# Kernel optimization log

Hardware: AMD Instinct MI355X
Metric: run time of the kernel (lower is better)

Reference implementation:

```python
import jax, jax.numpy as jnp
import numpy as np

PATCH = 13  # fixed patch_size -> rfft bins = 13//2 + 1 = 7


def setup_inputs() -> dict:
    key = jax.random.key(0)
    k1, k2, k3 = jax.random.split(key, 3)
    B, C, n, t = 32, 64, 128, PATCH
    embed_dim = 512
    x = jax.random.normal(k1, (B, C, n, t), dtype=jnp.float32)
    # Linear(patch_size//2+1 -> embed_dim): store weight as [in, out]
    W = jax.random.normal(k2, (t // 2 + 1, embed_dim), dtype=jnp.float32) * (1.0 / np.sqrt(t // 2 + 1))
    b = jax.random.normal(k3, (embed_dim,), dtype=jnp.float32) * 0.01
    return {"x": x, "W": W, "b": b}


def reference(x, W, b):
    # x: [B, C, n, t]; rfft with norm='forward' scales by 1/t.
    spec = jnp.fft.rfft(x, axis=-1, norm="forward")  # [B, C, n, t//2+1] complex
    mag = jnp.abs(spec).astype(x.dtype)               # [B, C, n, 7]
    # Linear + Dropout(0.1) in eval mode (identity)
    return jnp.einsum("bcnf,fe->bcne", mag, W) + b    # [B, C, n, embed_dim]
```

## Files before the change

kernel.cpp:

```cpp
#include <hip/hip_runtime.h>
#include <math.h>


constexpr int T = 13;
constexpr int F = 7;
constexpr int E = 512;
constexpr int ROWS = 128;

typedef float f4 __attribute__((ext_vector_type(4)));

__global__ __launch_bounds__(256, 8) void spectral_kernel(
    const float* __restrict__ x,
    const float* __restrict__ Wm,
    const float* __restrict__ bias,
    float* __restrict__ out)
{
    constexpr float CC[T] = {
         1.0f,
         0.8854560256532099f,  0.5680647467311558f,  0.1205366802553230f,
        -0.3546048870425356f, -0.7485107481711011f, -0.9709418174260520f,
        -0.9709418174260520f, -0.7485107481711011f, -0.3546048870425356f,
         0.1205366802553230f,  0.5680647467311558f,  0.8854560256532099f
    };
    constexpr float SS[T] = {
         0.0f,
         0.4647231720437686f,  0.8229838658936564f,  0.9927088740980540f,
         0.9350162426854148f,  0.6631226582407952f,  0.2393156642875578f,
        -0.2393156642875578f, -0.6631226582407952f, -0.9350162426854148f,
        -0.9927088740980540f, -0.8229838658936564f, -0.4647231720437686f
    };

    __shared__ float sx[ROWS * T];
    __shared__ float smag[F][ROWS];

    const int tid  = threadIdx.x;
    const int lane = tid & 63;
    const int wave = tid >> 6;
    const long long tile_base = (long long)blockIdx.x * ROWS;

    const float* __restrict__ xg = x + tile_base * T;
#pragma unroll
    for (int k = 0; k < 7; ++k) {
        const int idx = k * 256 + tid;
        if (idx < ROWS * T) sx[idx] = xg[idx];
    }
    __syncthreads();

    {
        const int row = tid & 127;
        float xv[T];
#pragma unroll
        for (int t = 0; t < T; ++t) xv[t] = sx[row * T + t];

        if (tid < 128) {
            float s = xv[0];
#pragma unroll
            for (int t = 1; t < T; ++t) s += xv[t];
            smag[0][row] = fabsf(s) * (1.0f / 13.0f);
#pragma unroll
            for (int f = 1; f < 4; ++f) {
                float re = xv[0], im = 0.0f;
#pragma unroll
                for (int t = 1; t < T; ++t) {
                    const int k = (f * t) % T;
                    re = fmaf(xv[t], CC[k], re);
                    im = fmaf(xv[t], SS[k], im);
                }
                smag[f][row] = sqrtf(fmaf(re, re, im * im)) * (1.0f / 13.0f);
            }
        } else {
#pragma unroll
            for (int f = 4; f < 7; ++f) {
                float re = xv[0], im = 0.0f;
#pragma unroll
                for (int t = 1; t < T; ++t) {
                    const int k = (f * t) % T;
                    re = fmaf(xv[t], CC[k], re);
                    im = fmaf(xv[t], SS[k], im);
                }
                smag[f][row] = sqrtf(fmaf(re, re, im * im)) * (1.0f / 13.0f);
            }
        }
    }
    __syncthreads();

    const int c0 = (wave & 1) * 256 + lane * 4;
    f4 wreg[F];
#pragma unroll
    for (int f = 0; f < F; ++f)
        wreg[f] = *reinterpret_cast<const f4*>(Wm + f * E + c0);
    const f4 breg = *reinterpret_cast<const f4*>(bias + c0);

    const int r0 = (wave >> 1) * 64;
    float* __restrict__ obase = out + (tile_base + r0) * (long long)E + c0;

#pragma unroll 2
    for (int r = 0; r < 64; ++r) {
        f4 a = breg;
#pragma unroll
        for (int f = 0; f < F; ++f) {
            const float m = smag[f][r0 + r];
            a.x = fmaf(m, wreg[f].x, a.x);
            a.y = fmaf(m, wreg[f].y, a.y);
            a.z = fmaf(m, wreg[f].z, a.z);
            a.w = fmaf(m, wreg[f].w, a.w);
        }
        __builtin_nontemporal_store(a, reinterpret_cast<f4*>(obase + (long long)r * E));
    }
}

extern "C" void kernel_launch(void* const* d_in, const int* in_sizes, int n_in,
                              void* d_out, int out_size, void* d_ws, size_t ws_size,
                              hipStream_t stream) {
    const float* x = (const float*)d_in[0];
    const float* W = (const float*)d_in[1];
    const float* b = (const float*)d_in[2];
    float* out = (float*)d_out;

    const int nrows = in_sizes[0] / T;
    const int blocks = nrows / ROWS;

    spectral_kernel<<<blocks, 256, 0, stream>>>(x, W, b, out);
}
```

Before: 102.8 us.

## Double rows per block and have each thread cover both column halves

Each block now handles 256 rows instead of 128. Every thread computes all seven spectral magnitudes for its own row rather than splitting the frequencies across two thread halves. In the output stage each wave owns 64 rows and writes both 256-column halves, so it keeps two sets of weights and bias in registers and issues two stores per row. The aim is fewer blocks, less redundant weight loading per output, and removal of the divergent branch, at the cost of more registers, lower occupancy (launch bounds 4) and a serial DFT per thread.

```diff
diff --git a/kernel.cpp b/kernel.cpp
--- a/kernel.cpp
+++ b/kernel.cpp
@@ -5,11 +5,11 @@
 constexpr int T = 13;
 constexpr int F = 7;
 constexpr int E = 512;
-constexpr int ROWS = 128;
+constexpr int ROWS = 256;
 
 typedef float f4 __attribute__((ext_vector_type(4)));
 
-__global__ __launch_bounds__(256, 8) void spectral_kernel(
+__global__ __launch_bounds__(256, 4) void spectral_kernel(
     const float* __restrict__ x,
     const float* __restrict__ Wm,
     const float* __restrict__ bias,
@@ -40,72 +40,65 @@
 
     const float* __restrict__ xg = x + tile_base * T;
 #pragma unroll
-    for (int k = 0; k < 7; ++k) {
-        const int idx = k * 256 + tid;
-        if (idx < ROWS * T) sx[idx] = xg[idx];
-    }
+    for (int k = 0; k < T; ++k)
+        sx[k * 256 + tid] = xg[k * 256 + tid];
     __syncthreads();
 
     {
-        const int row = tid & 127;
         float xv[T];
 #pragma unroll
-        for (int t = 0; t < T; ++t) xv[t] = sx[row * T + t];
+        for (int t = 0; t < T; ++t) xv[t] = sx[tid * T + t];
 
-        if (tid < 128) {
-            float s = xv[0];
+        float s = xv[0];
 #pragma unroll
-            for (int t = 1; t < T; ++t) s += xv[t];
-            smag[0][row] = fabsf(s) * (1.0f / 13.0f);
+        for (int t = 1; t < T; ++t) s += xv[t];
+        smag[0][tid] = fabsf(s) * (1.0f / 13.0f);
+
 #pragma unroll
-            for (int f = 1; f < 4; ++f) {
-                float re = xv[0], im = 0.0f;
+        for (int f = 1; f < F; ++f) {
+            float re = xv[0], im = 0.0f;
 #pragma unroll
-                for (int t = 1; t < T; ++t) {
-                    const int k = (f * t) % T;
-                    re = fmaf(xv[t], CC[k], re);
-                    im = fmaf(xv[t], SS[k], im);
-                }
-                smag[f][row] = sqrtf(fmaf(re, re, im * im)) * (1.0f / 13.0f);
+            for (int t = 1; t < T; ++t) {
+                const int k = (f * t) % T;
+                re = fmaf(xv[t], CC[k], re);
+                im = fmaf(xv[t], SS[k], im);
             }
-        } else {
-#pragma unroll
-            for (int f = 4; f < 7; ++f) {
-                float re = xv[0], im = 0.0f;
-#pragma unroll
-                for (int t = 1; t < T; ++t) {
-                    const int k = (f * t) % T;
-                    re = fmaf(xv[t], CC[k], re);
-                    im = fmaf(xv[t], SS[k], im);
-                }
-                smag[f][row] = sqrtf(fmaf(re, re, im * im)) * (1.0f / 13.0f);
-            }
+            smag[f][tid] = sqrtf(fmaf(re, re, im * im)) * (1.0f / 13.0f);
         }
     }
     __syncthreads();
 
-    const int c0 = (wave & 1) * 256 + lane * 4;
-    f4 wreg[F];
+    const int c0 = lane * 4;
+    f4 w0[F], w1[F];
 #pragma unroll
-    for (int f = 0; f < F; ++f)
-        wreg[f] = *reinterpret_cast<const f4*>(Wm + f * E + c0);
-    const f4 breg = *reinterpret_cast<const f4*>(bias + c0);
+    for (int f = 0; f < F; ++f) {
+        w0[f] = *reinterpret_cast<const f4*>(Wm + f * E + c0);
+        w1[f] = *reinterpret_cast<const f4*>(Wm + f * E + 256 + c0);
+    }
+    const f4 b0 = *reinterpret_cast<const f4*>(bias + c0);
+    const f4 b1 = *reinterpret_cast<const f4*>(bias + 256 + c0);
 
-    const int r0 = (wave >> 1) * 64;
+    const int r0 = wave * 64;
     float* __restrict__ obase = out + (tile_base + r0) * (long long)E + c0;
 
 #pragma unroll 2
     for (int r = 0; r < 64; ++r) {
-        f4 a = breg;
+        f4 a0 = b0, a1 = b1;
 #pragma unroll
         for (int f = 0; f < F; ++f) {
             const float m = smag[f][r0 + r];
-            a.x = fmaf(m, wreg[f].x, a.x);
-            a.y = fmaf(m, wreg[f].y, a.y);
-            a.z = fmaf(m, wreg[f].z, a.z);
-            a.w = fmaf(m, wreg[f].w, a.w);
+            a0.x = fmaf(m, w0[f].x, a0.x);
+            a0.y = fmaf(m, w0[f].y, a0.y);
+            a0.z = fmaf(m, w0[f].z, a0.z);
+            a0.w = fmaf(m, w0[f].w, a0.w);
+            a1.x = fmaf(m, w1[f].x, a1.x);
+            a1.y = fmaf(m, w1[f].y, a1.y);
+            a1.z = fmaf(m, w1[f].z, a1.z);
+            a1.w = fmaf(m, w1[f].w, a1.w);
         }
-        __builtin_nontemporal_store(a, reinterpret_cast<f4*>(obase + (long long)r * E));
+        __builtin_nontemporal_store(a0, reinterpret_cast<f4*>(obase));
+        __builtin_nontemporal_store(a1, reinterpret_cast<f4*>(obase + 256));
+        obase += E;
     }
 }
 
```

Result: no change. 103.3 us (+0.5%).
